# Kernel optimization log

Hardware: AMD Instinct MI355X
Metric: run time of the kernel (lower is better)

Reference implementation:

```python
import jax, jax.numpy as jnp
import numpy as np

JITTER = 0.01  # router_noise


def setup_inputs() -> dict:
    key = jax.random.key(0)
    ks = jax.random.split(key, 8)
    B, H, W, D = 4, 32, 64, 512
    E, F = 8, 2048
    N = B * H * W
    s = lambda fan: 1.0 / np.sqrt(fan)
    return {
        "input_data": jax.random.normal(ks[0], (B, H, W, D), dtype=jnp.float32),
        "attr": jax.random.normal(ks[1], (N, 3), dtype=jnp.float32),
        "Wr": jax.random.normal(ks[2], (3, E), dtype=jnp.float32) * s(3),
        "br": jnp.zeros((E,), dtype=jnp.float32),
        "W1": jax.random.normal(ks[3], (E, D, F), dtype=jnp.float32) * s(D),
        "b1": jnp.zeros((E, F), dtype=jnp.float32),
        "W2": jax.random.normal(ks[4], (E, F, D), dtype=jnp.float32) * s(F),
        "b2": jnp.zeros((E, D), dtype=jnp.float32),
    }


def reference(input_data, attr, Wr, br, W1, b1, W2, b2):
    B, H, W_, D = input_data.shape
    E = W1.shape[0]
    x = input_data.reshape(-1, D)  # [N, D]

    # --- Top1Router with multiplicative jitter noise in [1-eps, 1+eps] ---
    u = jax.random.uniform(jax.random.key(42), attr.shape, dtype=attr.dtype)
    noisy_attr = attr * ((1.0 + JITTER) - 2.0 * JITTER * u)
    router_logits = noisy_attr @ Wr + br                   # [N, E]
    router_probs = jax.nn.softmax(router_logits, axis=-1)  # [N, E]
    routes = jnp.argmax(router_probs, axis=-1)             # [N] int
    route_prob_max = jnp.max(router_probs, axis=-1)        # [N]

    # --- Dispatch to top-1 expert (eval: no capacity dropping) ---
    # Fixed small loop over experts; masked dense compute (jit-friendly,
    # no data-dependent shapes).
    out = jnp.zeros_like(x)
    for i in range(E):
        h = jax.nn.gelu(x @ W1[i] + b1[i], approximate=False)  # [N, F]
        y = h @ W2[i] + b2[i]                                  # [N, D]
        out = jnp.where((routes == i)[:, None], y, out)

    # is_scale_prob=True: scale output by the max routing probability
    out = out * route_prob_max[:, None]
    return out.reshape(B, H, W_, D)
```

## Files before the change

kernel.cpp:

```cpp
#include <hip/hip_runtime.h>
#include <hip/hip_bf16.h>

typedef unsigned int u32;
typedef __bf16 bf16x8 __attribute__((ext_vector_type(8)));
typedef float  f32x4  __attribute__((ext_vector_type(4)));

#define NTOK 8192
#define DIM  512
#define FDIM 2048
#define NEXP 8

#define OFF_W1T   0ull
#define OFF_W2T   16777216ull
#define OFF_XB    33554432ull
#define OFF_H     41943040ull
#define OFF_SCALE 75497472ull
#define OFF_CNT   75530240ull
#define OFF_LIST  75530272ull

__device__ __forceinline__ u32 rotl32(u32 x, int r) { return (x << r) | (x >> (32 - r)); }

__device__ __forceinline__ void threefry2x32(u32 k0, u32 k1, u32 x0, u32 x1,
                                             u32& y0, u32& y1) {
  u32 ks2 = k0 ^ k1 ^ 0x1BD11BDAu;
  x0 += k0; x1 += k1;
#define TF_RND(r) { x0 += x1; x1 = rotl32(x1, r); x1 ^= x0; }
  TF_RND(13) TF_RND(15) TF_RND(26) TF_RND(6)
  x0 += k1;  x1 += ks2 + 1u;
  TF_RND(17) TF_RND(29) TF_RND(16) TF_RND(24)
  x0 += ks2; x1 += k0 + 2u;
  TF_RND(13) TF_RND(15) TF_RND(26) TF_RND(6)
  x0 += k0;  x1 += k1 + 3u;
  TF_RND(17) TF_RND(29) TF_RND(16) TF_RND(24)
  x0 += k1;  x1 += ks2 + 4u;
  TF_RND(13) TF_RND(15) TF_RND(26) TF_RND(6)
  x0 += ks2; x1 += k0 + 5u;
#undef TF_RND
  y0 = x0; y1 = x1;
}

__device__ __forceinline__ float jax_uniform(u32 j) {
  u32 y0, y1;
  threefry2x32(0u, 42u, 0u, j, y0, y1);
  u32 bits = y0 ^ y1;
  return __uint_as_float((bits >> 9) | 0x3F800000u) - 1.0f;
}

__device__ __forceinline__ unsigned short f2b(float f) {
  u32 u = __float_as_uint(f);
  u32 r = (u + 0x7FFFu + ((u >> 16) & 1u)) >> 16;
  return (unsigned short)r;
}

__global__ __launch_bounds__(256) void router_kernel(
    const float* __restrict__ attr, const float* __restrict__ Wr,
    const float* __restrict__ br, float* __restrict__ scale,
    int* __restrict__ cnt, int* __restrict__ list) {
  int i = blockIdx.x * 256 + threadIdx.x;
  if (i >= NTOK) return;
  float a[3];
#pragma unroll
  for (int c = 0; c < 3; ++c) {
    float u = jax_uniform((u32)(3 * i + c));
    a[c] = attr[3 * i + c] * ((1.0f + 0.01f) - 2.0f * 0.01f * u);
  }
  float logits[NEXP];
#pragma unroll
  for (int e = 0; e < NEXP; ++e)
    logits[e] = br[e] + a[0] * Wr[0 * NEXP + e] + a[1] * Wr[1 * NEXP + e] + a[2] * Wr[2 * NEXP + e];
  float m = logits[0]; int am = 0;
#pragma unroll
  for (int e = 1; e < NEXP; ++e)
    if (logits[e] > m) { m = logits[e]; am = e; }
  float s = 0.f;
#pragma unroll
  for (int e = 0; e < NEXP; ++e) s += __expf(logits[e] - m) * 0.0f + expf(logits[e] - m);
  scale[i] = 1.0f / s;
  int pos = atomicAdd(&cnt[am], 1);
  list[am * NTOK + pos] = i;
}

__global__ __launch_bounds__(256) void convert_x_kernel(const float4* __restrict__ in,
                                                        uint2* __restrict__ out) {
  int i = blockIdx.x * 256 + threadIdx.x;
  if (i >= NTOK * DIM / 4) return;
  float4 v = in[i];
  u32 lo = (u32)f2b(v.x) | ((u32)f2b(v.y) << 16);
  u32 hi = (u32)f2b(v.z) | ((u32)f2b(v.w) << 16);
  out[i] = make_uint2(lo, hi);
}

__global__ __launch_bounds__(256) void transpose_bf16_kernel(
    const float* __restrict__ in, unsigned short* __restrict__ out, int R, int C) {
  int e = blockIdx.z;
  in  += (size_t)e * R * C;
  out += (size_t)e * R * C;
  __shared__ float tile[32][33];
  int c0 = blockIdx.x * 32, r0 = blockIdx.y * 32;
  int tr = threadIdx.x >> 5;
  int tc = threadIdx.x & 31;
#pragma unroll
  for (int it = 0; it < 4; ++it)
    tile[tr + it * 8][tc] = in[(size_t)(r0 + tr + it * 8) * C + c0 + tc];
  __syncthreads();
#pragma unroll
  for (int it = 0; it < 4; ++it)
    out[(size_t)(c0 + tr + it * 8) * R + r0 + tc] = f2b(tile[tc][tr + it * 8]);
}

__device__ __forceinline__ void load_lds16(const void* g, void* l) {
  __builtin_amdgcn_global_load_lds(
      (const __attribute__((address_space(1))) u32*)g,
      (__attribute__((address_space(3))) u32*)l, 16, 0, 0);
}

template <int KK, int NN, bool G1>
__global__ __launch_bounds__(256) void moe_gemm_kernel(
    const unsigned short* __restrict__ A,
    const unsigned short* __restrict__ Bt,
    const float* __restrict__ bias,
    const int* __restrict__ list,
    const int* __restrict__ cnt,
    const float* __restrict__ scale,
    unsigned short* __restrict__ Hout,
    float* __restrict__ Yout) {
  const int e = blockIdx.z;
  const int cn = cnt[e];
  const int m0 = blockIdx.y * 128;
  if (m0 >= cn) return;
  const int n0 = blockIdx.x * 128;
  const int tid = threadIdx.x;
  const int lane = tid & 63;
  const int wid = tid >> 6;
  const int wm = wid >> 1, wn = wid & 1;

  __shared__ unsigned short Asm[128 * 32];
  __shared__ unsigned short Bsm[128 * 32];

  const int* mylist = list + e * NTOK;
  const unsigned short* Be = Bt + (size_t)e * NN * KK;

  int aoff[2], boff[2], ldso[2];
#pragma unroll
  for (int j = 0; j < 2; ++j) {
    int o = j * 4096 + tid * 16;
    int row = o >> 6;
    int slot = (o >> 4) & 3;
    int g = (slot - (row >> 1)) & 3;
    int p = m0 + row; if (p >= cn) p = cn - 1;
    int tok = mylist[p];
    aoff[j] = tok * KK + g * 8;
    boff[j] = (n0 + row) * KK + g * 8;
    ldso[j] = o;
  }

  f32x4 acc[4][4];
#pragma unroll
  for (int i = 0; i < 4; ++i)
#pragma unroll
    for (int j = 0; j < 4; ++j) acc[i][j] = (f32x4){0.f, 0.f, 0.f, 0.f};

  int a_addr[4], b_addr[4];
#pragma unroll
  for (int mi = 0; mi < 4; ++mi) {
    int row = wm * 64 + mi * 16 + (lane & 15);
    int gp = ((lane >> 4) + (row >> 1)) & 3;
    a_addr[mi] = row * 32 + gp * 8;
  }
#pragma unroll
  for (int ni = 0; ni < 4; ++ni) {
    int row = wn * 64 + ni * 16 + (lane & 15);
    int gp = ((lane >> 4) + (row >> 1)) & 3;
    b_addr[ni] = row * 32 + gp * 8;
  }

  for (int kt = 0; kt < KK / 32; ++kt) {
#pragma unroll
    for (int j = 0; j < 2; ++j) {
      load_lds16(A + aoff[j] + kt * 32, (char*)Asm + ldso[j]);
      load_lds16(Be + boff[j] + kt * 32, (char*)Bsm + ldso[j]);
    }
    __syncthreads();
    bf16x8 af[4], bfr[4];
#pragma unroll
    for (int mi = 0; mi < 4; ++mi) af[mi] = *(const bf16x8*)(Asm + a_addr[mi]);
#pragma unroll
    for (int ni = 0; ni < 4; ++ni) bfr[ni] = *(const bf16x8*)(Bsm + b_addr[ni]);
#pragma unroll
    for (int mi = 0; mi < 4; ++mi)
#pragma unroll
      for (int ni = 0; ni < 4; ++ni)
        acc[mi][ni] = __builtin_amdgcn_mfma_f32_16x16x32_bf16(af[mi], bfr[ni], acc[mi][ni], 0, 0, 0);
    __syncthreads();
  }

  const int colb = n0 + wn * 64 + (lane & 15);
  float bia[4];
#pragma unroll
  for (int ni = 0; ni < 4; ++ni) bia[ni] = bias[(size_t)e * NN + colb + ni * 16];
#pragma unroll
  for (int mi = 0; mi < 4; ++mi) {
#pragma unroll
    for (int i = 0; i < 4; ++i) {
      int p = m0 + wm * 64 + mi * 16 + (lane >> 4) * 4 + i;
      if (p < cn) {
        int tok = mylist[p];
        if constexpr (G1) {
#pragma unroll
          for (int ni = 0; ni < 4; ++ni) {
            float v = acc[mi][ni][i] + bia[ni];
            float g = 0.5f * v * (1.0f + erff(v * 0.70710678118654752f));
            Hout[(size_t)tok * NN + colb + ni * 16] = f2b(g);
          }
        } else {
          float s = scale[tok];
#pragma unroll
          for (int ni = 0; ni < 4; ++ni) {
            float v = (acc[mi][ni][i] + bia[ni]) * s;
            Yout[(size_t)tok * NN + colb + ni * 16] = v;
          }
        }
      }
    }
  }
}

extern "C" void kernel_launch(void* const* d_in, const int* in_sizes, int n_in,
                              void* d_out, int out_size, void* d_ws, size_t ws_size,
                              hipStream_t stream) {
  const float* x    = (const float*)d_in[0];
  const float* attr = (const float*)d_in[1];
  const float* Wr   = (const float*)d_in[2];
  const float* br   = (const float*)d_in[3];
  const float* W1   = (const float*)d_in[4];
  const float* b1   = (const float*)d_in[5];
  const float* W2   = (const float*)d_in[6];
  const float* b2   = (const float*)d_in[7];
  float* out = (float*)d_out;
  char* ws = (char*)d_ws;

  unsigned short* W1t = (unsigned short*)(ws + OFF_W1T);
  unsigned short* W2t = (unsigned short*)(ws + OFF_W2T);
  unsigned short* xb  = (unsigned short*)(ws + OFF_XB);
  unsigned short* H   = (unsigned short*)(ws + OFF_H);
  float* scale        = (float*)(ws + OFF_SCALE);
  int* cnt            = (int*)(ws + OFF_CNT);
  int* list           = (int*)(ws + OFF_LIST);

  hipMemsetAsync(cnt, 0, NEXP * sizeof(int), stream);
  router_kernel<<<NTOK / 256, 256, 0, stream>>>(attr, Wr, br, scale, cnt, list);
  convert_x_kernel<<<(NTOK * DIM / 4) / 256, 256, 0, stream>>>((const float4*)x, (uint2*)xb);
  transpose_bf16_kernel<<<dim3(FDIM / 32, DIM / 32, NEXP), 256, 0, stream>>>(W1, W1t, DIM, FDIM);
  transpose_bf16_kernel<<<dim3(DIM / 32, FDIM / 32, NEXP), 256, 0, stream>>>(W2, W2t, FDIM, DIM);

  moe_gemm_kernel<DIM, FDIM, true><<<dim3(FDIM / 128, NTOK / 128, NEXP), 256, 0, stream>>>(
      xb, W1t, b1, list, cnt, scale, H, nullptr);
  moe_gemm_kernel<FDIM, DIM, false><<<dim3(DIM / 128, NTOK / 128, NEXP), 256, 0, stream>>>(
      H, W2t, b2, list, cnt, scale, nullptr, out);
}
```

Measured before the change: 189.0 us.

## Double-buffer LDS in MoE GEMM and split-K the second GEMM with atomics

The MoE GEMM now double-buffers its shared-memory tiles, so the global-to-LDS load for the next K step is issued before the MFMAs on the current one, and it requests 4 blocks per CU through launch bounds. The second GEMM (K=2048) is split into 4 K-chunks launched as extra grid-z blocks, and their partial results are combined into a zeroed output with float atomic adds. This targets load latency and the poor occupancy of the small-N second GEMM. In exchange it adds an output memset, atomic traffic and a nondeterministic summation order. It also removes a dead extra exp term in the router.

Result: slower. 209.5 us (+10.8%).

```diff
diff --git a/kernel.cpp b/kernel.cpp
--- a/kernel.cpp
+++ b/kernel.cpp
@@ -74,7 +74,7 @@
     if (logits[e] > m) { m = logits[e]; am = e; }
   float s = 0.f;
 #pragma unroll
-  for (int e = 0; e < NEXP; ++e) s += __expf(logits[e] - m) * 0.0f + expf(logits[e] - m);
+  for (int e = 0; e < NEXP; ++e) s += expf(logits[e] - m);
   scale[i] = 1.0f / s;
   int pos = atomicAdd(&cnt[am], 1);
   list[am * NTOK + pos] = i;
@@ -114,8 +114,8 @@
       (__attribute__((address_space(3))) u32*)l, 16, 0, 0);
 }
 
-template <int KK, int NN, bool G1>
-__global__ __launch_bounds__(256) void moe_gemm_kernel(
+template <int KK, int NN, bool G1, int SPLITK>
+__global__ __launch_bounds__(256, 4) void moe_gemm_kernel(
     const unsigned short* __restrict__ A,
     const unsigned short* __restrict__ Bt,
     const float* __restrict__ bias,
@@ -124,7 +124,8 @@
     const float* __restrict__ scale,
     unsigned short* __restrict__ Hout,
     float* __restrict__ Yout) {
-  const int e = blockIdx.z;
+  const int e = blockIdx.z % NEXP;
+  const int chunk = blockIdx.z / NEXP;
   const int cn = cnt[e];
   const int m0 = blockIdx.y * 128;
   if (m0 >= cn) return;
@@ -134,8 +135,11 @@
   const int wid = tid >> 6;
   const int wm = wid >> 1, wn = wid & 1;
 
-  __shared__ unsigned short Asm[128 * 32];
-  __shared__ unsigned short Bsm[128 * 32];
+  constexpr int KC = KK / SPLITK;
+  constexpr int NSTEP = KC / 32;
+  const int k_base = chunk * KC;
+
+  __shared__ __align__(16) unsigned short SM[2 * 8192];
 
   const int* mylist = list + e * NTOK;
   const unsigned short* Be = Bt + (size_t)e * NN * KK;
@@ -149,8 +153,8 @@
     int g = (slot - (row >> 1)) & 3;
     int p = m0 + row; if (p >= cn) p = cn - 1;
     int tok = mylist[p];
-    aoff[j] = tok * KK + g * 8;
-    boff[j] = (n0 + row) * KK + g * 8;
+    aoff[j] = tok * KK + g * 8 + k_base;
+    boff[j] = (n0 + row) * KK + g * 8 + k_base;
     ldso[j] = o;
   }
 
@@ -165,34 +169,53 @@
   for (int mi = 0; mi < 4; ++mi) {
     int row = wm * 64 + mi * 16 + (lane & 15);
     int gp = ((lane >> 4) + (row >> 1)) & 3;
-    a_addr[mi] = row * 32 + gp * 8;
+    a_addr[mi] = (row * 32 + gp * 8) * 2;
   }
 #pragma unroll
   for (int ni = 0; ni < 4; ++ni) {
     int row = wn * 64 + ni * 16 + (lane & 15);
     int gp = ((lane >> 4) + (row >> 1)) & 3;
-    b_addr[ni] = row * 32 + gp * 8;
-  }
-
-  for (int kt = 0; kt < KK / 32; ++kt) {
-#pragma unroll
-    for (int j = 0; j < 2; ++j) {
-      load_lds16(A + aoff[j] + kt * 32, (char*)Asm + ldso[j]);
-      load_lds16(Be + boff[j] + kt * 32, (char*)Bsm + ldso[j]);
-    }
+    b_addr[ni] = (row * 32 + gp * 8) * 2;
+  }
+
+#define STAGE(kt, b)                                                        \
+  {                                                                         \
+    int koff = (kt) * 32;                                                   \
+    char* base = (char*)SM + (b) * 16384;                                   \
+    _Pragma("unroll")                                                       \
+    for (int j = 0; j < 2; ++j) {                                           \
+      load_lds16(A + aoff[j] + koff, base + ldso[j]);                       \
+      load_lds16(Be + boff[j] + koff, base + 8192 + ldso[j]);               \
+    }                                                                       \
+  }
+
+#define COMPUTE(b)                                                          \
+  {                                                                         \
+    const char* base = (const char*)SM + (b) * 16384;                       \
+    bf16x8 af[4], bfr[4];                                                   \
+    _Pragma("unroll")                                                       \
+    for (int mi = 0; mi < 4; ++mi) af[mi] = *(const bf16x8*)(base + a_addr[mi]); \
+    _Pragma("unroll")                                                       \
+    for (int ni = 0; ni < 4; ++ni) bfr[ni] = *(const bf16x8*)(base + 8192 + b_addr[ni]); \
+    _Pragma("unroll")                                                       \
+    for (int mi = 0; mi < 4; ++mi)                                          \
+      _Pragma("unroll")                                                     \
+      for (int ni = 0; ni < 4; ++ni)                                        \
+        acc[mi][ni] = __builtin_amdgcn_mfma_f32_16x16x32_bf16(af[mi], bfr[ni], acc[mi][ni], 0, 0, 0); \
+  }
+
+  STAGE(0, 0)
+  __syncthreads();
+  int cur = 0;
+  for (int kt = 0; kt < NSTEP - 1; ++kt) {
+    STAGE(kt + 1, cur ^ 1)
+    COMPUTE(cur)
     __syncthreads();
-    bf16x8 af[4], bfr[4];
-#pragma unroll
-    for (int mi = 0; mi < 4; ++mi) af[mi] = *(const bf16x8*)(Asm + a_addr[mi]);
-#pragma unroll
-    for (int ni = 0; ni < 4; ++ni) bfr[ni] = *(const bf16x8*)(Bsm + b_addr[ni]);
-#pragma unroll
-    for (int mi = 0; mi < 4; ++mi)
-#pragma unroll
-      for (int ni = 0; ni < 4; ++ni)
-        acc[mi][ni] = __builtin_amdgcn_mfma_f32_16x16x32_bf16(af[mi], bfr[ni], acc[mi][ni], 0, 0, 0);
-    __syncthreads();
-  }
+    cur ^= 1;
+  }
+  COMPUTE(cur)
+#undef STAGE
+#undef COMPUTE
 
   const int colb = n0 + wn * 64 + (lane & 15);
   float bia[4];
@@ -216,8 +239,8 @@
           float s = scale[tok];
 #pragma unroll
           for (int ni = 0; ni < 4; ++ni) {
-            float v = (acc[mi][ni][i] + bia[ni]) * s;
-            Yout[(size_t)tok * NN + colb + ni * 16] = v;
+            float v = acc[mi][ni][i] + (chunk == 0 ? bia[ni] : 0.0f);
+            unsafeAtomicAdd(&Yout[(size_t)tok * NN + colb + ni * 16], v * s);
           }
         }
       }
@@ -248,13 +271,14 @@
   int* list           = (int*)(ws + OFF_LIST);
 
   hipMemsetAsync(cnt, 0, NEXP * sizeof(int), stream);
+  hipMemsetAsync(out, 0, (size_t)out_size * sizeof(float), stream);
   router_kernel<<<NTOK / 256, 256, 0, stream>>>(attr, Wr, br, scale, cnt, list);
   convert_x_kernel<<<(NTOK * DIM / 4) / 256, 256, 0, stream>>>((const float4*)x, (uint2*)xb);
   transpose_bf16_kernel<<<dim3(FDIM / 32, DIM / 32, NEXP), 256, 0, stream>>>(W1, W1t, DIM, FDIM);
   transpose_bf16_kernel<<<dim3(DIM / 32, FDIM / 32, NEXP), 256, 0, stream>>>(W2, W2t, FDIM, DIM);
 
-  moe_gemm_kernel<DIM, FDIM, true><<<dim3(FDIM / 128, NTOK / 128, NEXP), 256, 0, stream>>>(
+  moe_gemm_kernel<DIM, FDIM, true, 1><<<dim3(FDIM / 128, NTOK / 128, NEXP), 256, 0, stream>>>(
       xb, W1t, b1, list, cnt, scale, H, nullptr);
-  moe_gemm_kernel<FDIM, DIM, false><<<dim3(DIM / 128, NTOK / 128, NEXP), 256, 0, stream>>>(
+  moe_gemm_kernel<FDIM, DIM, false, 4><<<dim3(DIM / 128, NTOK / 128, NEXP * 4), 256, 0, stream>>>(
       H, W2t, b2, list, cnt, scale, nullptr, out);
 }
```
